# Kernel optimization log

Hardware: AMD Instinct MI355X
Metric: run time of the kernel (lower is better)

The kernel has to match this reference:

```python
import jax, jax.numpy as jnp
import numpy as np

EPS = 1e-5  # BatchNorm2d eps; BN in eval mode with running_mean=0, running_var=1

def conv_bn_relu(x, W, g, b):
    # x: [B, Cin, N, K]; W: [Cout, Cin] (1x1 conv). BN eval: (y-0)/sqrt(1+eps)*g + b, then ReLU.
    y = jnp.einsum('oc,bcnk->bonk', W, x)
    scale = (g / jnp.sqrt(1.0 + EPS))[None, :, None, None]
    return jax.nn.relu(y * scale + b[None, :, None, None])

def gather_neighbour(pc, idx):
    # pc: [B, N, d]; idx: [B, N, K] -> [B, N, K, d]
    B, N, K = idx.shape
    flat = idx.reshape(B, N * K, 1)
    return jnp.take_along_axis(pc, flat, axis=1).reshape(B, N, K, pc.shape[-1])

def setup_inputs() -> dict:
    B, N, K, D, H = 4, 40960, 16, 64, 32  # H = D // rfa_param
    key = jax.random.key(0)
    ks = jax.random.split(key, 16)
    inp = {
        'feature': jax.random.normal(ks[0], (B, D, N, 1), jnp.float32),
        'xyz': jax.random.normal(ks[1], (B, N, 3), jnp.float32),
        'neigh_idx': jax.random.randint(ks[2], (B, N, K), 0, N, jnp.int64),
        'W1': jax.random.normal(ks[3], (H, 10), jnp.float32) * 0.1,
        'W2': jax.random.normal(ks[4], (H, D), jnp.float32) * 0.1,
        'W3': jax.random.normal(ks[5], (H, 2 * H), jnp.float32) * 0.1,
        'W4': jax.random.normal(ks[6], (D, 2 * H), jnp.float32) * 0.1,
    }
    for i, h in zip(range(1, 5), (H, H, H, D)):
        inp[f'g{i}'] = jax.random.uniform(ks[6 + i], (h,), jnp.float32) + 0.5
        inp[f'b{i}'] = jax.random.normal(ks[10 + i], (h,), jnp.float32) * 0.1
    return inp

def reference(feature, xyz, W1, g1, b1, W2, g2, b2, W3, g3, b3, W4, g4, b4, neigh_idx):
    B, N, K = neigh_idx.shape
    # relative position encoding -> [B, N, K, 10]
    neighbor_xyz = gather_neighbour(xyz, neigh_idx)
    xyz_tile = jnp.broadcast_to(xyz[:, :, None, :], (B, N, K, 3))
    relative_xyz = xyz_tile - neighbor_xyz
    relative_dis = jnp.sqrt(jnp.sum(relative_xyz ** 2, axis=-1, keepdims=True))
    f_xyz = jnp.concatenate([relative_dis, relative_xyz, xyz_tile, neighbor_xyz], axis=-1)
    f_xyz = jnp.transpose(f_xyz, (0, 3, 1, 2))          # [B, 10, N, K]
    f_xyz = conv_bn_relu(f_xyz, W1, g1, b1)             # [B, H, N, K]
    f = conv_bn_relu(feature, W2, g2, b2)               # [B, H, N, 1]
    f_pts = jnp.transpose(f[..., 0], (0, 2, 1))         # [B, N, H]
    f_neighbours = gather_neighbour(f_pts, neigh_idx)   # [B, N, K, H]
    f_neighbours = jnp.transpose(f_neighbours, (0, 3, 1, 2))  # [B, H, N, K]
    f_concat = jnp.concatenate([f_neighbours, f_xyz], axis=1)  # [B, 2H, N, K]
    f_concat = conv_bn_relu(f_concat, W3, g3, b3)       # [B, H, N, K]
    f_concat = jnp.max(f_concat, axis=3, keepdims=True)  # max pooling over neighbors
    f = jnp.concatenate([f_concat, f], axis=1)          # [B, 2H, N, 1]
    return conv_bn_relu(f, W4, g4, b4)                  # [B, D, N, 1]
```

## Files before the change

### kernel.cpp

```cpp
#include <hip/hip_runtime.h>
#include <math.h>

typedef __bf16 bf16_t;
typedef bf16_t bf16x8 __attribute__((ext_vector_type(8)));
typedef bf16_t bf16x4 __attribute__((ext_vector_type(4)));
typedef float  f32x4  __attribute__((ext_vector_type(4)));
typedef int    intx4  __attribute__((ext_vector_type(4)));

#define MFMA16(a, b, c) __builtin_amdgcn_mfma_f32_16x16x32_bf16(a, b, c, 0, 0, 0)

constexpr float BN_INV = 0.999995000037499687f;

__global__ __launch_bounds__(256) void rfa_k1(
    const float* __restrict__ feature, const float* __restrict__ xyz,
    const float* __restrict__ W2,
    const float* __restrict__ g2, const float* __restrict__ b2,
    bf16_t* __restrict__ fbf, float4* __restrict__ xyz4,
    int N, int nwaves)
{
    int gtid = blockIdx.x * 256 + threadIdx.x;
    int w = gtid >> 6, lane = gtid & 63;
    if (w >= nwaves) return;
    int pt = lane & 15, quad = lane >> 4;
    int T0 = w * 64;
    int b  = T0 / N;
    int n0 = T0 - b * N;

    {
        size_t p = (size_t)T0 + lane;
        xyz4[p] = make_float4(xyz[p * 3], xyz[p * 3 + 1], xyz[p * 3 + 2], 0.f);
    }

    bf16x8 A[2][2];
    #pragma unroll
    for (int mt = 0; mt < 2; ++mt) {
        int h = mt * 16 + pt;
        float sc = g2[h] * BN_INV;
        #pragma unroll
        for (int ks = 0; ks < 2; ++ks) {
            const float* src = W2 + h * 64 + ks * 32 + quad * 8;
            bf16x8 v;
            #pragma unroll
            for (int j = 0; j < 8; ++j) v[j] = (bf16_t)(src[j] * sc);
            A[mt][ks] = v;
        }
    }
    float b2r[8];
    #pragma unroll
    for (int mt = 0; mt < 2; ++mt)
        #pragma unroll
        for (int r = 0; r < 4; ++r) b2r[mt * 4 + r] = b2[mt * 16 + quad * 4 + r];

    const float* fb = feature + (size_t)b * 64 * N;

    #pragma unroll
    for (int g = 0; g < 4; ++g) {
        int nn = n0 + g * 16 + pt;
        size_t T = (size_t)T0 + g * 16 + pt;
        bf16x8 Bf[2];
        #pragma unroll
        for (int ks = 0; ks < 2; ++ks) {
            bf16x8 v;
            #pragma unroll
            for (int j = 0; j < 8; ++j)
                v[j] = (bf16_t)fb[(size_t)(ks * 32 + quad * 8 + j) * N + nn];
            Bf[ks] = v;
        }
        f32x4 acc[2] = {f32x4{0,0,0,0}, f32x4{0,0,0,0}};
        #pragma unroll
        for (int mt = 0; mt < 2; ++mt) {
            acc[mt] = MFMA16(A[mt][0], Bf[0], acc[mt]);
            acc[mt] = MFMA16(A[mt][1], Bf[1], acc[mt]);
        }
        #pragma unroll
        for (int mt = 0; mt < 2; ++mt) {
            bf16x4 o;
            #pragma unroll
            for (int r = 0; r < 4; ++r)
                o[r] = (bf16_t)fmaxf(acc[mt][r] + b2r[mt * 4 + r], 0.f);
            *(bf16x4*)(fbf + T * 32 + mt * 16 + quad * 4) = o;
        }
    }
}

__global__ __launch_bounds__(256) void rfa_k2(
    const bf16_t* __restrict__ fbf, const float4* __restrict__ xyz4,
    const int* __restrict__ nidx,
    const float* __restrict__ W1, const float* __restrict__ g1, const float* __restrict__ b1,
    const float* __restrict__ W3, const float* __restrict__ g3, const float* __restrict__ b3,
    const float* __restrict__ W4, const float* __restrict__ g4, const float* __restrict__ b4,
    float* __restrict__ out, int N)
{
    __shared__ __align__(16) bf16_t sW4[8 * 64 * 8];
    __shared__ float sB[4][32 * 18];
    __shared__ __align__(16) float sb3[32];

    int tid = threadIdx.x;
    for (int s = tid; s < 512; s += 256) {
        int f = s >> 6, l = s & 63;
        int mt = f >> 1, ks = f & 1, nn = l & 15, q = l >> 4;
        int o = mt * 16 + nn;
        float sc = g4[o] * BN_INV;
        const float* src = W4 + o * 64 + ks * 32 + q * 8;
        bf16x8 v;
        #pragma unroll
        for (int j = 0; j < 8; ++j) v[j] = (bf16_t)(src[j] * sc);
        *(bf16x8*)(sW4 + s * 8) = v;
    }
    if (tid < 32) sb3[tid] = b3[tid];
    __syncthreads();

    int lane = tid & 63, wv = tid >> 6;
    int n = lane & 15, quad = lane >> 4;

    int blk   = blockIdx.x;
    int b     = (blk & 7) >> 1;
    int slot  = (blk >> 3) * 2 + (blk & 1);
    int BPB   = gridDim.x >> 2;
    int WPB   = BPB * 4;
    int wslot = wv * BPB + slot;
    int GPB   = N >> 4;
    int base  = b * N;

    bf16x8 A3[2][2];
    #pragma unroll
    for (int mt = 0; mt < 2; ++mt) {
        int h = mt * 16 + n;
        float sc = g3[h] * BN_INV;
        #pragma unroll
        for (int ks = 0; ks < 2; ++ks) {
            const float* src = W3 + h * 64 + ks * 32 + quad * 8;
            bf16x8 v;
            #pragma unroll
            for (int j = 0; j < 8; ++j) v[j] = (bf16_t)(src[j] * sc);
            A3[mt][ks] = v;
        }
    }
    float a8[8], V0[8], V1[8], V2[8];
    #pragma unroll
    for (int j = 0; j < 8; ++j) {
        int c = quad * 8 + j;
        float s1 = g1[c] * BN_INV;
        const float* wp = W1 + c * 10;
        a8[j] = wp[0] * s1;
        V0[j] = (wp[7] - wp[1]) * s1;
        V1[j] = (wp[8] - wp[2]) * s1;
        V2[j] = (wp[9] - wp[3]) * s1;
    }

    const bf16_t* fb  = fbf  + (size_t)base * 32;
    const float4* xzb = xyz4 + (size_t)base;
    float* bounce = sB[wv];

    for (int grp = wslot; grp < GPB; grp += WPB) {
        int nloc = grp * 16;
        size_t tg = (size_t)base + nloc + n;

        float4 ps = xyz4[tg];
        float hoist[8];
        #pragma unroll
        for (int j = 0; j < 8; ++j) {
            int c = quad * 8 + j;
            float s1 = g1[c] * BN_INV;
            const float* wp = W1 + c * 10;
            hoist[j] = b1[c] + ((wp[1] + wp[4]) * ps.x + (wp[2] + wp[5]) * ps.y +
                                (wp[3] + wp[6]) * ps.z) * s1;
        }

        const int* nb = nidx + tg * 16;
        intx4 nc0 = __builtin_nontemporal_load((const intx4*)(nb + 0));
        intx4 nc1 = __builtin_nontemporal_load((const intx4*)(nb + 4));

        bf16x8 fj[4]; float4 pn[4];
        #pragma unroll
        for (int s = 0; s < 4; ++s) {
            int j0 = nc0[s];
            fj[s] = *(const bf16x8*)(fb + (size_t)j0 * 32 + quad * 8);
            pn[s] = xzb[j0];
        }
        nc0 = __builtin_nontemporal_load((const intx4*)(nb + 8));

        f32x4 mx0 = {-3.0e38f, -3.0e38f, -3.0e38f, -3.0e38f};
        f32x4 mx1 = {-3.0e38f, -3.0e38f, -3.0e38f, -3.0e38f};

        #pragma unroll
        for (int k = 0; k < 16; ++k) {
            int s = k & 3;
            float4 p = pn[s];
            bf16x8 Bj = fj[s];

            float rx = ps.x - p.x, ry = ps.y - p.y, rz = ps.z - p.z;
            float dist = __builtin_amdgcn_sqrtf(rx * rx + ry * ry + rz * rz);

            bf16x8 Bx;
            #pragma unroll
            for (int c = 0; c < 8; ++c) {
                float v = fmaf(a8[c], dist, hoist[c]);
                v = fmaf(V0[c], p.x, v);
                v = fmaf(V1[c], p.y, v);
                v = fmaf(V2[c], p.z, v);
                Bx[c] = (bf16_t)fmaxf(v, 0.f);
            }

            f32x4 ac0 = {0,0,0,0}, ac1 = {0,0,0,0};
            ac0 = MFMA16(A3[0][0], Bj, ac0);
            ac0 = MFMA16(A3[0][1], Bx, ac0);
            ac1 = MFMA16(A3[1][0], Bj, ac1);
            ac1 = MFMA16(A3[1][1], Bx, ac1);
            #pragma unroll
            for (int r = 0; r < 4; ++r) {
                mx0[r] = fmaxf(mx0[r], ac0[r]);
                mx1[r] = fmaxf(mx1[r], ac1[r]);
            }

            if (k + 4 < 16) {
                int t = k + 4;
                int jn;
                if      (t < 8)  jn = nc1[t - 4];
                else if (t < 12) jn = nc0[t - 8];
                else             jn = nc1[t - 12];
                fj[s] = *(const bf16x8*)(fb + (size_t)jn * 32 + quad * 8);
                pn[s] = xzb[jn];
            }
            if (k == 3) nc1 = __builtin_nontemporal_load((const intx4*)(nb + 12));
        }

        f32x4 bz0 = *(const f32x4*)&sb3[quad * 4];
        f32x4 bz1 = *(const f32x4*)&sb3[16 + quad * 4];
        #pragma unroll
        for (int r = 0; r < 4; ++r) {
            bounce[(quad * 4 + r) * 18 + n]      = fmaxf(mx0[r] + bz0[r], 0.f);
            bounce[(16 + quad * 4 + r) * 18 + n] = fmaxf(mx1[r] + bz1[r], 0.f);
        }
        asm volatile("s_waitcnt lgkmcnt(0)" ::: "memory");
        bf16x8 Bm;
        #pragma unroll
        for (int jj = 0; jj < 8; ++jj)
            Bm[jj] = (bf16_t)bounce[(quad * 8 + jj) * 18 + n];

        bf16x8 Bs = *(const bf16x8*)(fb + (size_t)(nloc + n) * 32 + quad * 8);

        #pragma unroll
        for (int mt = 0; mt < 4; ++mt) {
            bf16x8 A40 = *(const bf16x8*)(sW4 + ((size_t)(mt * 2 + 0) * 64 + lane) * 8);
            bf16x8 A41 = *(const bf16x8*)(sW4 + ((size_t)(mt * 2 + 1) * 64 + lane) * 8);
            f32x4 acc = {0,0,0,0};
            acc = MFMA16(A40, Bm, acc);
            acc = MFMA16(A41, Bs, acc);
            #pragma unroll
            for (int r = 0; r < 4; ++r) {
                int o = mt * 16 + quad * 4 + r;
                float res = fmaxf(acc[r] + b4[o], 0.f);
                __builtin_nontemporal_store(res, &out[((size_t)b * 64 + o) * N + nloc + n]);
            }
        }
        asm volatile("s_waitcnt lgkmcnt(0)" ::: "memory");
    }
}

extern "C" void kernel_launch(void* const* d_in, const int* in_sizes, int n_in,
                              void* d_out, int out_size, void* d_ws, size_t ws_size,
                              hipStream_t stream) {
    const float* feature = (const float*)d_in[0];
    const float* xyz     = (const float*)d_in[1];
    const int*   nidx    = (const int*)  d_in[2];
    const float* W1      = (const float*)d_in[3];
    const float* W2      = (const float*)d_in[4];
    const float* W3      = (const float*)d_in[5];
    const float* W4      = (const float*)d_in[6];
    const float* g1 = (const float*)d_in[7];
    const float* b1 = (const float*)d_in[8];
    const float* g2 = (const float*)d_in[9];
    const float* b2 = (const float*)d_in[10];
    const float* g3 = (const float*)d_in[11];
    const float* b3 = (const float*)d_in[12];
    const float* g4 = (const float*)d_in[13];
    const float* b4 = (const float*)d_in[14];
    float* out = (float*)d_out;

    const int B = 4;
    const int N = in_sizes[1] / (B * 3);
    const int total = B * N;

    bf16_t* fbf  = (bf16_t*)d_ws;
    float4* xyz4 = (float4*)((char*)d_ws + (size_t)total * 32 * sizeof(bf16_t));

    const int nw1 = total / 64;
    const int blk1 = (nw1 + 3) / 4;
    const int blk2 = 1024;

    rfa_k1<<<blk1, 256, 0, stream>>>(feature, xyz, W2, g2, b2, fbf, xyz4, N, nw1);
    rfa_k2<<<blk2, 256, 0, stream>>>(fbf, xyz4, nidx, W1, g1, b1, W3, g3, b3,
                                     W4, g4, b4, out, N);
}
```

Before: 182.3 us.

## Software-pipeline neighbor gathers across groups and stage b4 bias in LDS

The neighbor-index loads, query point xyz, and the first four neighbor feature/position gathers for the next group are now issued inside the current group's k-loop. This hides the gather latency at the start of each group that previously stalled the wave. The b4 bias is also copied into shared memory and read as a vector, instead of being loaded from global memory once per output element. The cost is more live registers and redundant gathers on the last iteration, where the same group is reloaded.

```diff
diff --git a/kernel.cpp b/kernel.cpp
--- a/kernel.cpp
+++ b/kernel.cpp
@@ -8,6 +8,7 @@
 typedef int    intx4  __attribute__((ext_vector_type(4)));
 
 #define MFMA16(a, b, c) __builtin_amdgcn_mfma_f32_16x16x32_bf16(a, b, c, 0, 0, 0)
+#define NTL(p) __builtin_nontemporal_load((const intx4*)(p))
 
 constexpr float BN_INV = 0.999995000037499687f;
 
@@ -93,7 +94,7 @@
 {
     __shared__ __align__(16) bf16_t sW4[8 * 64 * 8];
     __shared__ float sB[4][32 * 18];
-    __shared__ __align__(16) float sb3[32];
+    __shared__ __align__(16) float sb34[96];
 
     int tid = threadIdx.x;
     for (int s = tid; s < 512; s += 256) {
@@ -107,7 +108,8 @@
         for (int j = 0; j < 8; ++j) v[j] = (bf16_t)(src[j] * sc);
         *(bf16x8*)(sW4 + s * 8) = v;
     }
-    if (tid < 32) sb3[tid] = b3[tid];
+    if (tid < 32) sb34[tid] = b3[tid];
+    else if (tid < 96) sb34[tid] = b4[tid - 32];
     __syncthreads();
 
     int lane = tid & 63, wv = tid >> 6;
@@ -152,11 +154,30 @@
     const float4* xzb = xyz4 + (size_t)base;
     float* bounce = sB[wv];
 
+    size_t tg = (size_t)base + (size_t)wslot * 16 + n;
+    const int* nb = nidx + tg * 16;
+    intx4 c1, c2;
+    float4 ps;
+    bf16x8 fj[4]; float4 pn[4];
+    {
+        intx4 c0 = NTL(nb + 0);
+        c1 = NTL(nb + 4);
+        ps = xyz4[tg];
+        #pragma unroll
+        for (int s = 0; s < 4; ++s) {
+            int j0 = c0[s];
+            fj[s] = *(const bf16x8*)(fb + (size_t)j0 * 32 + quad * 8);
+            pn[s] = xzb[j0];
+        }
+        c2 = NTL(nb + 8);
+    }
+
     for (int grp = wslot; grp < GPB; grp += WPB) {
-        int nloc = grp * 16;
-        size_t tg = (size_t)base + nloc + n;
-
-        float4 ps = xyz4[tg];
+        int  nloc = grp * 16;
+        bool hn   = (grp + WPB) < GPB;
+        size_t tgN = hn ? tg + (size_t)WPB * 16 : tg;
+        const int* nbN = nidx + tgN * 16;
+
         float hoist[8];
         #pragma unroll
         for (int j = 0; j < 8; ++j) {
@@ -167,21 +188,10 @@
                                 (wp[3] + wp[6]) * ps.z) * s1;
         }
 
-        const int* nb = nidx + tg * 16;
-        intx4 nc0 = __builtin_nontemporal_load((const intx4*)(nb + 0));
-        intx4 nc1 = __builtin_nontemporal_load((const intx4*)(nb + 4));
-
-        bf16x8 fj[4]; float4 pn[4];
-        #pragma unroll
-        for (int s = 0; s < 4; ++s) {
-            int j0 = nc0[s];
-            fj[s] = *(const bf16x8*)(fb + (size_t)j0 * 32 + quad * 8);
-            pn[s] = xzb[j0];
-        }
-        nc0 = __builtin_nontemporal_load((const intx4*)(nb + 8));
-
         f32x4 mx0 = {-3.0e38f, -3.0e38f, -3.0e38f, -3.0e38f};
         f32x4 mx1 = {-3.0e38f, -3.0e38f, -3.0e38f, -3.0e38f};
+        intx4 c3, cA;
+        float4 psN;
 
         #pragma unroll
         for (int k = 0; k < 16; ++k) {
@@ -213,20 +223,24 @@
                 mx1[r] = fmaxf(mx1[r], ac1[r]);
             }
 
-            if (k + 4 < 16) {
-                int t = k + 4;
+            {
                 int jn;
-                if      (t < 8)  jn = nc1[t - 4];
-                else if (t < 12) jn = nc0[t - 8];
-                else             jn = nc1[t - 12];
+                if      (k < 4)  jn = c1[k];
+                else if (k < 8)  jn = c2[k - 4];
+                else if (k < 12) jn = c3[k - 8];
+                else             jn = cA[k - 12];
                 fj[s] = *(const bf16x8*)(fb + (size_t)jn * 32 + quad * 8);
                 pn[s] = xzb[jn];
             }
-            if (k == 3) nc1 = __builtin_nontemporal_load((const intx4*)(nb + 12));
-        }
-
-        f32x4 bz0 = *(const f32x4*)&sb3[quad * 4];
-        f32x4 bz1 = *(const f32x4*)&sb3[16 + quad * 4];
+            if (k == 2)  c3 = NTL(nb + 12);
+            if (k == 4)  cA = NTL(nbN + 0);
+            if (k == 8)  c1 = NTL(nbN + 4);
+            if (k == 12) psN = xyz4[tgN];
+            if (k == 13) c2 = NTL(nbN + 8);
+        }
+
+        f32x4 bz0 = *(const f32x4*)&sb34[quad * 4];
+        f32x4 bz1 = *(const f32x4*)&sb34[16 + quad * 4];
         #pragma unroll
         for (int r = 0; r < 4; ++r) {
             bounce[(quad * 4 + r) * 18 + n]      = fmaxf(mx0[r] + bz0[r], 0.f);
@@ -244,17 +258,20 @@
         for (int mt = 0; mt < 4; ++mt) {
             bf16x8 A40 = *(const bf16x8*)(sW4 + ((size_t)(mt * 2 + 0) * 64 + lane) * 8);
             bf16x8 A41 = *(const bf16x8*)(sW4 + ((size_t)(mt * 2 + 1) * 64 + lane) * 8);
+            f32x4 b4q = *(const f32x4*)&sb34[32 + mt * 16 + quad * 4];
             f32x4 acc = {0,0,0,0};
             acc = MFMA16(A40, Bm, acc);
             acc = MFMA16(A41, Bs, acc);
             #pragma unroll
             for (int r = 0; r < 4; ++r) {
                 int o = mt * 16 + quad * 4 + r;
-                float res = fmaxf(acc[r] + b4[o], 0.f);
+                float res = fmaxf(acc[r] + b4q[r], 0.f);
                 __builtin_nontemporal_store(res, &out[((size_t)b * 64 + o) * N + nloc + n]);
             }
         }
         asm volatile("s_waitcnt lgkmcnt(0)" ::: "memory");
+
+        tg = tgN; nb = nbN; ps = psN;
     }
 }
 
```

Measured after the change: 182.8 us. About the same (+0.3%).

## Move W1 coefficients and biases to LDS, drop nontemporal index loads, raise grid

Applied to the files above, without the earlier changes.

Per-lane W1-derived coefficient arrays (32 VGPRs) are moved into shared memory and re-read through volatile vector LDS loads inside the neighbour loop, which cuts register pressure so more waves can stay resident. The b4 bias is also staged in LDS instead of being read from global memory for every output. Neighbour-index loads become ordinary cached loads rather than nontemporal ones, and the second kernel's grid grows from 1024 to 1280 blocks. The cost is extra LDS traffic in the innermost loop, and the larger grid may no longer divide the work evenly across waves.

```diff
diff --git a/kernel.cpp b/kernel.cpp
--- a/kernel.cpp
+++ b/kernel.cpp
@@ -93,7 +93,8 @@
 {
     __shared__ __align__(16) bf16_t sW4[8 * 64 * 8];
     __shared__ float sB[4][32 * 18];
-    __shared__ __align__(16) float sb3[32];
+    __shared__ __align__(16) float sV[128];
+    __shared__ __align__(16) float sb34[96];
 
     int tid = threadIdx.x;
     for (int s = tid; s < 512; s += 256) {
@@ -107,7 +108,18 @@
         for (int j = 0; j < 8; ++j) v[j] = (bf16_t)(src[j] * sc);
         *(bf16x8*)(sW4 + s * 8) = v;
     }
-    if (tid < 32) sb3[tid] = b3[tid];
+    if (tid < 32) {
+        int c = tid;
+        float s1 = g1[c] * BN_INV;
+        const float* wp = W1 + c * 10;
+        sV[c]      = wp[0] * s1;
+        sV[32 + c] = (wp[7] - wp[1]) * s1;
+        sV[64 + c] = (wp[8] - wp[2]) * s1;
+        sV[96 + c] = (wp[9] - wp[3]) * s1;
+        sb34[c] = b3[c];
+    } else if (tid >= 64 && tid < 128) {
+        sb34[tid - 32] = b4[tid - 64];
+    }
     __syncthreads();
 
     int lane = tid & 63, wv = tid >> 6;
@@ -136,21 +148,14 @@
             A3[mt][ks] = v;
         }
     }
-    float a8[8], V0[8], V1[8], V2[8];
-    #pragma unroll
-    for (int j = 0; j < 8; ++j) {
-        int c = quad * 8 + j;
-        float s1 = g1[c] * BN_INV;
-        const float* wp = W1 + c * 10;
-        a8[j] = wp[0] * s1;
-        V0[j] = (wp[7] - wp[1]) * s1;
-        V1[j] = (wp[8] - wp[2]) * s1;
-        V2[j] = (wp[9] - wp[3]) * s1;
-    }
 
     const bf16_t* fb  = fbf  + (size_t)base * 32;
     const float4* xzb = xyz4 + (size_t)base;
     float* bounce = sB[wv];
+    volatile const f32x4* vA  = (volatile const f32x4*)&sV[0  + quad * 8];
+    volatile const f32x4* vV0 = (volatile const f32x4*)&sV[32 + quad * 8];
+    volatile const f32x4* vV1 = (volatile const f32x4*)&sV[64 + quad * 8];
+    volatile const f32x4* vV2 = (volatile const f32x4*)&sV[96 + quad * 8];
 
     for (int grp = wslot; grp < GPB; grp += WPB) {
         int nloc = grp * 16;
@@ -168,8 +173,8 @@
         }
 
         const int* nb = nidx + tg * 16;
-        intx4 nc0 = __builtin_nontemporal_load((const intx4*)(nb + 0));
-        intx4 nc1 = __builtin_nontemporal_load((const intx4*)(nb + 4));
+        intx4 nc0 = *(const intx4*)(nb + 0);
+        intx4 nc1 = *(const intx4*)(nb + 4);
 
         bf16x8 fj[4]; float4 pn[4];
         #pragma unroll
@@ -178,7 +183,7 @@
             fj[s] = *(const bf16x8*)(fb + (size_t)j0 * 32 + quad * 8);
             pn[s] = xzb[j0];
         }
-        nc0 = __builtin_nontemporal_load((const intx4*)(nb + 8));
+        nc0 = *(const intx4*)(nb + 8);
 
         f32x4 mx0 = {-3.0e38f, -3.0e38f, -3.0e38f, -3.0e38f};
         f32x4 mx1 = {-3.0e38f, -3.0e38f, -3.0e38f, -3.0e38f};
@@ -194,12 +199,19 @@
 
             bf16x8 Bx;
             #pragma unroll
-            for (int c = 0; c < 8; ++c) {
-                float v = fmaf(a8[c], dist, hoist[c]);
-                v = fmaf(V0[c], p.x, v);
-                v = fmaf(V1[c], p.y, v);
-                v = fmaf(V2[c], p.z, v);
-                Bx[c] = (bf16_t)fmaxf(v, 0.f);
+            for (int hf = 0; hf < 2; ++hf) {
+                f32x4 aa = vA[hf];
+                f32x4 w0 = vV0[hf];
+                f32x4 w1 = vV1[hf];
+                f32x4 w2 = vV2[hf];
+                #pragma unroll
+                for (int c = 0; c < 4; ++c) {
+                    float v = fmaf(aa[c], dist, hoist[hf * 4 + c]);
+                    v = fmaf(w0[c], p.x, v);
+                    v = fmaf(w1[c], p.y, v);
+                    v = fmaf(w2[c], p.z, v);
+                    Bx[hf * 4 + c] = (bf16_t)fmaxf(v, 0.f);
+                }
             }
 
             f32x4 ac0 = {0,0,0,0}, ac1 = {0,0,0,0};
@@ -222,11 +234,11 @@
                 fj[s] = *(const bf16x8*)(fb + (size_t)jn * 32 + quad * 8);
                 pn[s] = xzb[jn];
             }
-            if (k == 3) nc1 = __builtin_nontemporal_load((const intx4*)(nb + 12));
-        }
-
-        f32x4 bz0 = *(const f32x4*)&sb3[quad * 4];
-        f32x4 bz1 = *(const f32x4*)&sb3[16 + quad * 4];
+            if (k == 3) nc1 = *(const intx4*)(nb + 12);
+        }
+
+        f32x4 bz0 = *(const f32x4*)&sb34[quad * 4];
+        f32x4 bz1 = *(const f32x4*)&sb34[16 + quad * 4];
         #pragma unroll
         for (int r = 0; r < 4; ++r) {
             bounce[(quad * 4 + r) * 18 + n]      = fmaxf(mx0[r] + bz0[r], 0.f);
@@ -244,13 +256,14 @@
         for (int mt = 0; mt < 4; ++mt) {
             bf16x8 A40 = *(const bf16x8*)(sW4 + ((size_t)(mt * 2 + 0) * 64 + lane) * 8);
             bf16x8 A41 = *(const bf16x8*)(sW4 + ((size_t)(mt * 2 + 1) * 64 + lane) * 8);
+            f32x4 b4q = *(const f32x4*)&sb34[32 + mt * 16 + quad * 4];
             f32x4 acc = {0,0,0,0};
             acc = MFMA16(A40, Bm, acc);
             acc = MFMA16(A41, Bs, acc);
             #pragma unroll
             for (int r = 0; r < 4; ++r) {
                 int o = mt * 16 + quad * 4 + r;
-                float res = fmaxf(acc[r] + b4[o], 0.f);
+                float res = fmaxf(acc[r] + b4q[r], 0.f);
                 __builtin_nontemporal_store(res, &out[((size_t)b * 64 + o) * N + nloc + n]);
             }
         }
@@ -287,7 +300,7 @@
 
     const int nw1 = total / 64;
     const int blk1 = (nw1 + 3) / 4;
-    const int blk2 = 1024;
+    const int blk2 = 1280;
 
     rfa_k1<<<blk1, 256, 0, stream>>>(feature, xyz, W2, g2, b2, fbf, xyz4, N, nw1);
     rfa_k2<<<blk2, 256, 0, stream>>>(fbf, xyz4, nidx, W1, g1, b1, W3, g3, b3,
```

After: 208.6 us. +14.4%, slower.

## Compress gathered xyz to fp16 and neighbour indices to 16-bit

Applied to the files above, without the earlier changes.

The first kernel now packs xyz into fp16x4 (8 bytes per point) and packs neighbour indices into 16-bit pairs. The second kernel reads these compact forms, so each gathered xyz and each index load moves fewer bytes. Indices become 32-bit unsigned offsets, b4 is staged in shared memory, and the grid grows from 1024 to 1280 blocks. The risks are precision loss from fp16 coordinates and 16-bit indices that only hold while N stays below 65536, as in the test. The first kernel also still reads the full int index array once, so that traffic moves rather than disappears.

```diff
diff --git a/kernel.cpp b/kernel.cpp
--- a/kernel.cpp
+++ b/kernel.cpp
@@ -6,6 +6,9 @@
 typedef bf16_t bf16x4 __attribute__((ext_vector_type(4)));
 typedef float  f32x4  __attribute__((ext_vector_type(4)));
 typedef int    intx4  __attribute__((ext_vector_type(4)));
+typedef unsigned int uintx4 __attribute__((ext_vector_type(4)));
+typedef _Float16 h16;
+typedef h16 h16x4 __attribute__((ext_vector_type(4)));
 
 #define MFMA16(a, b, c) __builtin_amdgcn_mfma_f32_16x16x32_bf16(a, b, c, 0, 0, 0)
 
@@ -13,9 +16,11 @@
 
 __global__ __launch_bounds__(256) void rfa_k1(
     const float* __restrict__ feature, const float* __restrict__ xyz,
+    const int* __restrict__ nidx,
     const float* __restrict__ W2,
     const float* __restrict__ g2, const float* __restrict__ b2,
-    bf16_t* __restrict__ fbf, float4* __restrict__ xyz4,
+    bf16_t* __restrict__ fbf, h16x4* __restrict__ xyzh,
+    unsigned int* __restrict__ n16,
     int N, int nwaves)
 {
     int gtid = blockIdx.x * 256 + threadIdx.x;
@@ -28,7 +33,25 @@
 
     {
         size_t p = (size_t)T0 + lane;
-        xyz4[p] = make_float4(xyz[p * 3], xyz[p * 3 + 1], xyz[p * 3 + 2], 0.f);
+        h16x4 h; h[0] = (h16)xyz[p * 3]; h[1] = (h16)xyz[p * 3 + 1];
+        h[2] = (h16)xyz[p * 3 + 2]; h[3] = (h16)0.f;
+        xyzh[p] = h;
+        const int* np_ = nidx + p * 16;
+        intx4 a0 = *(const intx4*)(np_ + 0);
+        intx4 a1 = *(const intx4*)(np_ + 4);
+        intx4 a2 = *(const intx4*)(np_ + 8);
+        intx4 a3 = *(const intx4*)(np_ + 12);
+        uintx4 w0, w1;
+        w0[0] = (unsigned)a0[0] | ((unsigned)a0[1] << 16);
+        w0[1] = (unsigned)a0[2] | ((unsigned)a0[3] << 16);
+        w0[2] = (unsigned)a1[0] | ((unsigned)a1[1] << 16);
+        w0[3] = (unsigned)a1[2] | ((unsigned)a1[3] << 16);
+        w1[0] = (unsigned)a2[0] | ((unsigned)a2[1] << 16);
+        w1[1] = (unsigned)a2[2] | ((unsigned)a2[3] << 16);
+        w1[2] = (unsigned)a3[0] | ((unsigned)a3[1] << 16);
+        w1[3] = (unsigned)a3[2] | ((unsigned)a3[3] << 16);
+        *(uintx4*)(n16 + p * 8)     = w0;
+        *(uintx4*)(n16 + p * 8 + 4) = w1;
     }
 
     bf16x8 A[2][2];
@@ -84,8 +107,8 @@
 }
 
 __global__ __launch_bounds__(256) void rfa_k2(
-    const bf16_t* __restrict__ fbf, const float4* __restrict__ xyz4,
-    const int* __restrict__ nidx,
+    const bf16_t* __restrict__ fbf, const h16x4* __restrict__ xyzh,
+    const unsigned int* __restrict__ n16,
     const float* __restrict__ W1, const float* __restrict__ g1, const float* __restrict__ b1,
     const float* __restrict__ W3, const float* __restrict__ g3, const float* __restrict__ b3,
     const float* __restrict__ W4, const float* __restrict__ g4, const float* __restrict__ b4,
@@ -93,7 +116,7 @@
 {
     __shared__ __align__(16) bf16_t sW4[8 * 64 * 8];
     __shared__ float sB[4][32 * 18];
-    __shared__ __align__(16) float sb3[32];
+    __shared__ __align__(16) float sb34[96];
 
     int tid = threadIdx.x;
     for (int s = tid; s < 512; s += 256) {
@@ -107,7 +130,8 @@
         for (int j = 0; j < 8; ++j) v[j] = (bf16_t)(src[j] * sc);
         *(bf16x8*)(sW4 + s * 8) = v;
     }
-    if (tid < 32) sb3[tid] = b3[tid];
+    if (tid < 32) sb34[tid] = b3[tid];
+    else if (tid < 96) sb34[tid] = b4[tid - 32];
     __syncthreads();
 
     int lane = tid & 63, wv = tid >> 6;
@@ -148,37 +172,44 @@
         V2[j] = (wp[9] - wp[3]) * s1;
     }
 
-    const bf16_t* fb  = fbf  + (size_t)base * 32;
-    const float4* xzb = xyz4 + (size_t)base;
+    const bf16_t*       fb   = fbf  + (size_t)base * 32;
+    const h16x4*        xzb  = xyzh + (size_t)base;
+    const unsigned int* n16b = n16  + (size_t)base * 8;
+    float*              outb = out  + (size_t)base * 64;
     float* bounce = sB[wv];
 
+    #define IDX(t) ((t) < 8 ? (((t) & 1) ? (iw0[(t) >> 1] >> 16)              \
+                                         : (iw0[(t) >> 1] & 0xffffu))         \
+                            : (((t) & 1) ? (iw1[((t) - 8) >> 1] >> 16)        \
+                                         : (iw1[((t) - 8) >> 1] & 0xffffu)))
+
     for (int grp = wslot; grp < GPB; grp += WPB) {
-        int nloc = grp * 16;
-        size_t tg = (size_t)base + nloc + n;
-
-        float4 ps = xyz4[tg];
+        unsigned int nloc = (unsigned)grp * 16u;
+        unsigned int t32  = nloc + (unsigned)n;
+
+        uintx4 iw0 = *(const uintx4*)(n16b + (size_t)t32 * 8);
+        uintx4 iw1 = *(const uintx4*)(n16b + (size_t)t32 * 8 + 4);
+
+        h16x4 psh = xzb[t32];
+        float psx = (float)psh[0], psy = (float)psh[1], psz = (float)psh[2];
+
         float hoist[8];
         #pragma unroll
         for (int j = 0; j < 8; ++j) {
             int c = quad * 8 + j;
             float s1 = g1[c] * BN_INV;
             const float* wp = W1 + c * 10;
-            hoist[j] = b1[c] + ((wp[1] + wp[4]) * ps.x + (wp[2] + wp[5]) * ps.y +
-                                (wp[3] + wp[6]) * ps.z) * s1;
-        }
-
-        const int* nb = nidx + tg * 16;
-        intx4 nc0 = __builtin_nontemporal_load((const intx4*)(nb + 0));
-        intx4 nc1 = __builtin_nontemporal_load((const intx4*)(nb + 4));
-
-        bf16x8 fj[4]; float4 pn[4];
+            hoist[j] = b1[c] + ((wp[1] + wp[4]) * psx + (wp[2] + wp[5]) * psy +
+                                (wp[3] + wp[6]) * psz) * s1;
+        }
+
+        bf16x8 fj[4]; h16x4 pn[4];
         #pragma unroll
         for (int s = 0; s < 4; ++s) {
-            int j0 = nc0[s];
-            fj[s] = *(const bf16x8*)(fb + (size_t)j0 * 32 + quad * 8);
+            unsigned int j0 = IDX(s);
+            fj[s] = *(const bf16x8*)(fb + j0 * 32u + quad * 8u);
             pn[s] = xzb[j0];
         }
-        nc0 = __builtin_nontemporal_load((const intx4*)(nb + 8));
 
         f32x4 mx0 = {-3.0e38f, -3.0e38f, -3.0e38f, -3.0e38f};
         f32x4 mx1 = {-3.0e38f, -3.0e38f, -3.0e38f, -3.0e38f};
@@ -186,19 +217,20 @@
         #pragma unroll
         for (int k = 0; k < 16; ++k) {
             int s = k & 3;
-            float4 p = pn[s];
+            h16x4 p = pn[s];
             bf16x8 Bj = fj[s];
-
-            float rx = ps.x - p.x, ry = ps.y - p.y, rz = ps.z - p.z;
+            float pnx = (float)p[0], pny = (float)p[1], pnz = (float)p[2];
+
+            float rx = psx - pnx, ry = psy - pny, rz = psz - pnz;
             float dist = __builtin_amdgcn_sqrtf(rx * rx + ry * ry + rz * rz);
 
             bf16x8 Bx;
             #pragma unroll
             for (int c = 0; c < 8; ++c) {
                 float v = fmaf(a8[c], dist, hoist[c]);
-                v = fmaf(V0[c], p.x, v);
-                v = fmaf(V1[c], p.y, v);
-                v = fmaf(V2[c], p.z, v);
+                v = fmaf(V0[c], pnx, v);
+                v = fmaf(V1[c], pny, v);
+                v = fmaf(V2[c], pnz, v);
                 Bx[c] = (bf16_t)fmaxf(v, 0.f);
             }
 
@@ -214,19 +246,14 @@
             }
 
             if (k + 4 < 16) {
-                int t = k + 4;
-                int jn;
-                if      (t < 8)  jn = nc1[t - 4];
-                else if (t < 12) jn = nc0[t - 8];
-                else             jn = nc1[t - 12];
-                fj[s] = *(const bf16x8*)(fb + (size_t)jn * 32 + quad * 8);
+                unsigned int jn = IDX(k + 4);
+                fj[s] = *(const bf16x8*)(fb + jn * 32u + quad * 8u);
                 pn[s] = xzb[jn];
             }
-            if (k == 3) nc1 = __builtin_nontemporal_load((const intx4*)(nb + 12));
-        }
-
-        f32x4 bz0 = *(const f32x4*)&sb3[quad * 4];
-        f32x4 bz1 = *(const f32x4*)&sb3[16 + quad * 4];
+        }
+
+        f32x4 bz0 = *(const f32x4*)&sb34[quad * 4];
+        f32x4 bz1 = *(const f32x4*)&sb34[16 + quad * 4];
         #pragma unroll
         for (int r = 0; r < 4; ++r) {
             bounce[(quad * 4 + r) * 18 + n]      = fmaxf(mx0[r] + bz0[r], 0.f);
@@ -238,24 +265,26 @@
         for (int jj = 0; jj < 8; ++jj)
             Bm[jj] = (bf16_t)bounce[(quad * 8 + jj) * 18 + n];
 
-        bf16x8 Bs = *(const bf16x8*)(fb + (size_t)(nloc + n) * 32 + quad * 8);
+        bf16x8 Bs = *(const bf16x8*)(fb + t32 * 32u + quad * 8u);
 
         #pragma unroll
         for (int mt = 0; mt < 4; ++mt) {
             bf16x8 A40 = *(const bf16x8*)(sW4 + ((size_t)(mt * 2 + 0) * 64 + lane) * 8);
             bf16x8 A41 = *(const bf16x8*)(sW4 + ((size_t)(mt * 2 + 1) * 64 + lane) * 8);
+            f32x4 b4q = *(const f32x4*)&sb34[32 + mt * 16 + quad * 4];
             f32x4 acc = {0,0,0,0};
             acc = MFMA16(A40, Bm, acc);
             acc = MFMA16(A41, Bs, acc);
             #pragma unroll
             for (int r = 0; r < 4; ++r) {
-                int o = mt * 16 + quad * 4 + r;
-                float res = fmaxf(acc[r] + b4[o], 0.f);
-                __builtin_nontemporal_store(res, &out[((size_t)b * 64 + o) * N + nloc + n]);
+                unsigned int o = mt * 16 + quad * 4 + r;
+                float res = fmaxf(acc[r] + b4q[r], 0.f);
+                __builtin_nontemporal_store(res, outb + o * (unsigned)N + t32);
             }
         }
         asm volatile("s_waitcnt lgkmcnt(0)" ::: "memory");
     }
+    #undef IDX
 }
 
 extern "C" void kernel_launch(void* const* d_in, const int* in_sizes, int n_in,
@@ -282,14 +311,17 @@
     const int N = in_sizes[1] / (B * 3);
     const int total = B * N;
 
-    bf16_t* fbf  = (bf16_t*)d_ws;
-    float4* xyz4 = (float4*)((char*)d_ws + (size_t)total * 32 * sizeof(bf16_t));
+    bf16_t* fbf = (bf16_t*)d_ws;
+    h16x4*  xyzh = (h16x4*)((char*)d_ws + (size_t)total * 64);
+    unsigned int* n16 = (unsigned int*)((char*)d_ws + (size_t)total * 64
+                                        + (size_t)total * 8);
 
     const int nw1 = total / 64;
     const int blk1 = (nw1 + 3) / 4;
-    const int blk2 = 1024;
-
-    rfa_k1<<<blk1, 256, 0, stream>>>(feature, xyz, W2, g2, b2, fbf, xyz4, N, nw1);
-    rfa_k2<<<blk2, 256, 0, stream>>>(fbf, xyz4, nidx, W1, g1, b1, W3, g3, b3,
+    const int blk2 = 1280;
+
+    rfa_k1<<<blk1, 256, 0, stream>>>(feature, xyz, nidx, W2, g2, b2,
+                                     fbf, xyzh, n16, N, nw1);
+    rfa_k2<<<blk2, 256, 0, stream>>>(fbf, xyzh, n16, W1, g1, b1, W3, g3, b3,
                                      W4, g4, b4, out, N);
 }
```

New measurement: 198.5 us. 1.09x slower.
